# Performance work log

Measured on AMD Instinct MI355X. Metric: run time of the kernel, lower is better.

Reference implementation:

```python
import jax, jax.numpy as jnp
import numpy as np

HIDDEN = 2048
NUM_HEADS = 16
HEAD_DIM = HIDDEN // NUM_HEADS
INIT_RANGE = 0.02


def setup_inputs() -> dict:
    key = jax.random.key(0)
    ks = jax.random.split(key, 5)
    B, S = 2, 2048
    hidden_states = jax.random.normal(ks[0], (B, S, HIDDEN), dtype=jnp.float32)
    # Linear weights stored torch-style [out, in]; biases zero-init per _init_weights
    def w(k):
        return INIT_RANGE * jax.random.normal(k, (HIDDEN, HIDDEN), dtype=jnp.float32)
    return {
        "hidden_states": hidden_states,
        "wq": w(ks[1]), "bq": jnp.zeros((HIDDEN,), jnp.float32),
        "wk": w(ks[2]), "bk": jnp.zeros((HIDDEN,), jnp.float32),
        "wv": w(ks[3]), "bv": jnp.zeros((HIDDEN,), jnp.float32),
        "wo": w(ks[4]), "bo": jnp.zeros((HIDDEN,), jnp.float32),
    }


def _split_heads(x):
    # [B,S,H] -> [B,nh,S,hd]
    B, S, _ = x.shape
    return x.reshape(B, S, NUM_HEADS, HEAD_DIM).transpose(0, 2, 1, 3)


def reference(hidden_states, wq, bq, wk, bk, wv, bv, wo, bo):
    B, S, H = hidden_states.shape
    scale = 1.0 / np.sqrt(HEAD_DIM).astype(np.float32)

    q = _split_heads(hidden_states @ wq.T + bq)  # [B,nh,S,hd]
    k = _split_heads(hidden_states @ wk.T + bk)
    v = _split_heads(hidden_states @ wv.T + bv)

    attn = jnp.einsum('bhqd,bhkd->bhqk', q, k) * scale  # [B,nh,S,S]
    # causal mask: -inf above diagonal, 0 on/below
    causal = jnp.where(
        jnp.tril(jnp.ones((S, S), dtype=bool)),
        jnp.float32(0.0), jnp.float32(-jnp.inf))
    attn = attn + causal
    probs = jax.nn.softmax(attn, axis=-1)
    out = jnp.einsum('bhqk,bhkd->bhqd', probs, v)  # [B,nh,S,hd]
    out = out.transpose(0, 2, 1, 3).reshape(B, S, H)  # merge heads
    return out @ wo.T + bo
```

## Files before the change

kernel.cpp:

```cpp
#include <hip/hip_runtime.h>
#include <stdint.h>

typedef unsigned short u16;
typedef __attribute__((ext_vector_type(8))) short short8;
typedef __attribute__((ext_vector_type(4))) short short4v;
typedef __attribute__((ext_vector_type(4))) float float4v;

union V8u { short8 v; short4v h[2]; u16 u[8]; unsigned w[4]; };

__device__ __forceinline__ u16 f2bf(float f) {
  unsigned u = __float_as_uint(f);
  u = u + 0x7FFFu + ((u >> 16) & 1u);
  return (u16)(u >> 16);
}
__device__ __forceinline__ float4v fzero() {
  float4v z = {0.f, 0.f, 0.f, 0.f};
  return z;
}
__device__ __forceinline__ void gl_lds16(const u16* g, u16* l) {
  __builtin_amdgcn_global_load_lds(
      (const __attribute__((address_space(1))) void*)g,
      (__attribute__((address_space(3))) void*)l, 16, 0, 0);
}

#define MFMA16(a, b, c) __builtin_amdgcn_mfma_f32_16x16x32_bf16((a), (b), (c), 0, 0, 0)

__global__ void conv5_f32_bf16(const float* __restrict__ X,
                               const float* __restrict__ w0,
                               const float* __restrict__ w1,
                               const float* __restrict__ w2,
                               u16* __restrict__ dst, long seg) {
  const int y = blockIdx.y;
  const float* s = (y < 2) ? (X + (long)y * seg)
                           : (y == 2 ? w0 : (y == 3 ? w1 : w2));
  u16* d = dst + (long)y * seg;
  const long i = ((long)blockIdx.x * 256 + threadIdx.x) * 8;
  if (i >= seg) return;
  float4 a = *(const float4*)&s[i];
  float4 b = *(const float4*)&s[i + 4];
  V8u o;
  o.u[0] = f2bf(a.x); o.u[1] = f2bf(a.y); o.u[2] = f2bf(a.z); o.u[3] = f2bf(a.w);
  o.u[4] = f2bf(b.x); o.u[5] = f2bf(b.y); o.u[6] = f2bf(b.z); o.u[7] = f2bf(b.w);
  *(short8*)&d[i] = o.v;
}

__global__ void conv_f32_bf16(const float* __restrict__ in, u16* __restrict__ out, long n) {
  const long i = ((long)blockIdx.x * 256 + threadIdx.x) * 8;
  if (i >= n) return;
  float4 a = *(const float4*)&in[i];
  float4 b = *(const float4*)&in[i + 4];
  V8u o;
  o.u[0] = f2bf(a.x); o.u[1] = f2bf(a.y); o.u[2] = f2bf(a.z); o.u[3] = f2bf(a.w);
  o.u[4] = f2bf(b.x); o.u[5] = f2bf(b.y); o.u[6] = f2bf(b.z); o.u[7] = f2bf(b.w);
  *(short8*)&out[i] = o.v;
}

template <int NREP, bool OUTF32>
__global__ __launch_bounds__(512, 2) void gemm_bal(
    const u16* __restrict__ X, const u16* __restrict__ Wb,
    const float* __restrict__ b0, const float* __restrict__ b1,
    const float* __restrict__ b2, void* __restrict__ Out,
    int K, int cpx)
{
  constexpr int NH = NREP / 2;
  __shared__ __align__(16) u16 lds[2][(2 + NREP) * 4096];

  const int t = threadIdx.x;
  const int lane = t & 63;
  const int wave = t >> 6;
  const int quad = lane >> 4, l16 = lane & 15;
  const int wm = wave >> 2, wn = wave & 3;

  const int bid = (int)blockIdx.x;
  const int swz = (bid & 7) * cpx + (bid >> 3);
  const int by = swz & 31;
  const int bx = swz >> 5;
  const long m0 = (long)by * 128;
  const long n0 = (long)bx * (64 * NREP);

  const u16* pA[2];
  #pragma unroll
  for (int l = 0; l < 2; ++l) {
    const int d = l * 8192 + t * 16;
    const int o = d ^ ((d >> 3) & 0x70);
    pA[l] = X + (m0 + (o >> 7)) * (long)K + ((o & 127) >> 1);
  }
  const u16* pB[NREP];
  #pragma unroll
  for (int s = 0; s < NREP; ++s) {
    const int d = s * 8192 + t * 16;
    const int o = d ^ ((d >> 3) & 0x70);
    pB[s] = Wb + (n0 + (o >> 7)) * (long)K + ((o & 127) >> 1);
  }

  int offk[2];
  #pragma unroll
  for (int kk = 0; kk < 2; ++kk)
    offk[kk] = l16 * 128 + ((kk * 64 + quad * 16) ^ ((l16 & 7) << 4));

  float4v acc[4][NREP];
  #pragma unroll
  for (int i = 0; i < 4; ++i)
    #pragma unroll
    for (int j = 0; j < NREP; ++j) acc[i][j] = fzero();

  auto STAGE = [&](u16* Lb, int kt_) {
    #pragma unroll
    for (int l = 0; l < 2; ++l)
      gl_lds16(pA[l] + (long)kt_ * 64, Lb + l * 4096 + t * 8);
    #pragma unroll
    for (int s = 0; s < NREP; ++s)
      gl_lds16(pB[s] + (long)kt_ * 64, Lb + 8192 + s * 4096 + t * 8);
  };

#define SB() __builtin_amdgcn_sched_barrier(0)
#define BAR() do { asm volatile("s_barrier" ::: "memory"); SB(); } while (0)

  const int NT = K >> 6;

  STAGE(&lds[0][0], 0);
  asm volatile("s_waitcnt vmcnt(0)" ::: "memory");
  BAR();

  for (int kt = 0; kt < NT; ++kt) {
    const int buf = kt & 1;
    const int nkt = (kt + 1 < NT) ? kt + 1 : NT - 1;
    const char* Ab = (const char*)&lds[buf][0] + wm * 8192;
    const char* Bb = (const char*)&lds[buf][8192] + wn * (16 * NREP) * 128;

    short8 a[4][2], b[NREP][2];

    STAGE(&lds[buf ^ 1][0], nkt);

    #pragma unroll
    for (int i = 0; i < 4; ++i)
      a[i][0] = *(const short8*)(Ab + i * 2048 + offk[0]);
    #pragma unroll
    for (int j = 0; j < NH; ++j)
      b[j][0] = *(const short8*)(Bb + j * 2048 + offk[0]);
    #pragma unroll
    for (int j = NH; j < NREP; ++j)
      b[j][0] = *(const short8*)(Bb + j * 2048 + offk[0]);
    #pragma unroll
    for (int i = 0; i < 4; ++i)
      a[i][1] = *(const short8*)(Ab + i * 2048 + offk[1]);
    SB();

    __builtin_amdgcn_s_setprio(1);
    #pragma unroll
    for (int i = 0; i < 4; ++i)
      #pragma unroll
      for (int j = 0; j < NH; ++j)
        acc[i][j] = MFMA16(a[i][0], b[j][0], acc[i][j]);
    __builtin_amdgcn_s_setprio(0);
    SB();

    #pragma unroll
    for (int j = 0; j < NH; ++j)
      b[j][1] = *(const short8*)(Bb + j * 2048 + offk[1]);
    SB();

    __builtin_amdgcn_s_setprio(1);
    #pragma unroll
    for (int i = 0; i < 4; ++i)
      #pragma unroll
      for (int j = NH; j < NREP; ++j)
        acc[i][j] = MFMA16(a[i][0], b[j][0], acc[i][j]);
    __builtin_amdgcn_s_setprio(0);
    SB();

    #pragma unroll
    for (int j = NH; j < NREP; ++j)
      b[j][1] = *(const short8*)(Bb + j * 2048 + offk[1]);
    SB();

    __builtin_amdgcn_s_setprio(1);
    #pragma unroll
    for (int i = 0; i < 4; ++i)
      #pragma unroll
      for (int j = 0; j < NH; ++j)
        acc[i][j] = MFMA16(a[i][1], b[j][1], acc[i][j]);
    __builtin_amdgcn_s_setprio(0);
    SB();

    __builtin_amdgcn_s_setprio(1);
    #pragma unroll
    for (int i = 0; i < 4; ++i)
      #pragma unroll
      for (int j = NH; j < NREP; ++j)
        acc[i][j] = MFMA16(a[i][1], b[j][1], acc[i][j]);
    __builtin_amdgcn_s_setprio(0);

    asm volatile("s_waitcnt vmcnt(0)" ::: "memory");
    BAR();
  }

#undef SB
#undef BAR

  #pragma unroll
  for (int j = 0; j < NREP; ++j) {
    const int cg = (int)n0 + wn * (16 * NREP) + j * 16 + l16;
    const int z = cg >> 11, col = cg & 2047;
    const float* Bp = (z == 0) ? b0 : (z == 1 ? b1 : b2);
    const float bvv = Bp[col];
    #pragma unroll
    for (int i = 0; i < 4; ++i) {
      const long r0 = m0 + wm * 64 + i * 16 + quad * 4;
      #pragma unroll
      for (int r = 0; r < 4; ++r) {
        const long off = (long)z * (4096L * 2048) + (r0 + r) * 2048 + col;
        const float v = acc[i][j][r] + bvv;
        if (OUTF32) ((float*)Out)[off] = v;
        else        ((u16*)Out)[off] = f2bf(v);
      }
    }
  }
}

#define S_LEN 2048
#define HID   2048
#define HD    128

__global__ __launch_bounds__(256, 2) void attn_fwd(
    const u16* __restrict__ Q, const u16* __restrict__ K,
    const u16* __restrict__ V, u16* __restrict__ Ctx)
{
  __shared__ u16 Ks[2][32 * 136];
  __shared__ unsigned Vt[2][128 * 17];
  __shared__ u16 Ps[4 * 2 * 512];

  const int t = threadIdx.x;
  const int lane = t & 63, wave = t >> 6;
  const int quad = lane >> 4, l16 = lane & 15;
  const int b = blockIdx.y >> 4, h = blockIdx.y & 15;

  const long base = (long)b * S_LEN * HID + (long)h * HD;
  const u16* Qp = Q + base;
  const u16* Kp = K + base;
  const u16* Vp = V + base;
  u16* Cp = Ctx + base;

  const int sr2 = t >> 4;
  const int sc8 = (t & 15) * 8;

  short8 onesv;
  {
    V8u ou;
    #pragma unroll
    for (int j = 0; j < 8; ++j) ou.u[j] = 0x3F80;
    onesv = ou.v;
  }
  const float SC = 0.08838834764831845f * 1.4426950408889634f;

  for (int pass = 0; pass < 2; ++pass) {
    const int qb = (pass ? (int)blockIdx.x : 15 - (int)blockIdx.x) * 128;
    const int wqb = qb + wave * 32;

    short8 qf[2][4];
    #pragma unroll
    for (int g = 0; g < 2; ++g) {
      const long qr = wqb + g * 16 + l16;
      #pragma unroll
      for (int kk = 0; kk < 4; ++kk)
        qf[g][kk] = *(const short8*)&Qp[qr * HID + kk * 32 + quad * 8];
    }

    float4v o[2][9];
    #pragma unroll
    for (int g = 0; g < 2; ++g)
      #pragma unroll
      for (int i = 0; i < 9; ++i) o[g][i] = fzero();

    short8 kr0, kr1, vv0, vv1;
    {
      const long g = (long)(2 * sr2) * HID + sc8;
      kr0 = *(const short8*)&Kp[g];
      kr1 = *(const short8*)&Kp[g + HID];
      vv0 = *(const short8*)&Vp[g];
      vv1 = *(const short8*)&Vp[g + HID];
    }
    {
      *(short8*)&Ks[0][(2 * sr2) * 136 + sc8]     = kr0;
      *(short8*)&Ks[0][(2 * sr2 + 1) * 136 + sc8] = kr1;
      V8u a, c; a.v = vv0; c.v = vv1;
      #pragma unroll
      for (int j = 0; j < 8; ++j)
        Vt[0][(sc8 + j) * 17 + sr2] = (unsigned)a.u[j] | ((unsigned)c.u[j] << 16);
    }
    __syncthreads();

    const int T = (qb + 128) >> 5;
    for (int ti = 0; ti < T; ++ti) {
      const int kv0 = ti << 5;
      const int p = ti & 1;

      const bool more = (ti + 1 < T);
      if (more) {
        const long g = (long)(kv0 + 32 + 2 * sr2) * HID + sc8;
        kr0 = *(const short8*)&Kp[g];
        kr1 = *(const short8*)&Kp[g + HID];
        vv0 = *(const short8*)&Vp[g];
        vv1 = *(const short8*)&Vp[g + HID];
      }

      if (kv0 <= wqb) {
        float4v s[2][2];
        #pragma unroll
        for (int g = 0; g < 2; ++g) { s[g][0] = fzero(); s[g][1] = fzero(); }
        #pragma unroll
        for (int ni = 0; ni < 2; ++ni)
          #pragma unroll
          for (int kk = 0; kk < 4; ++kk) {
            short8 kf = *(const short8*)&Ks[p][(ni * 16 + l16) * 136 + kk * 32 + quad * 8];
            s[0][ni] = MFMA16(qf[0][kk], kf, s[0][ni]);
            s[1][ni] = MFMA16(qf[1][kk], kf, s[1][ni]);
          }

        const int pb = wave * 1024;
        #pragma unroll
        for (int g = 0; g < 2; ++g) {
          const int qrow0 = wqb + g * 16 + quad * 4;
          #pragma unroll
          for (int r = 0; r < 4; ++r) {
            float s0 = fminf(s[g][0][r] * SC, 80.f);
            float s1 = fminf(s[g][1][r] * SC, 80.f);
            if (kv0 + l16 > qrow0 + r)      s0 = -1e30f;
            if (kv0 + 16 + l16 > qrow0 + r) s1 = -1e30f;
            Ps[pb + g * 512 + (quad * 4 + r) * 32 + l16]      = f2bf(__builtin_amdgcn_exp2f(s0));
            Ps[pb + g * 512 + (quad * 4 + r) * 32 + 16 + l16] = f2bf(__builtin_amdgcn_exp2f(s1));
          }
        }
        __threadfence_block();
        short8 pf0 = *(const short8*)&Ps[pb + l16 * 32 + quad * 8];
        short8 pf1 = *(const short8*)&Ps[pb + 512 + l16 * 32 + quad * 8];

        #pragma unroll
        for (int dt = 0; dt < 8; ++dt) {
          const unsigned* vp = &Vt[p][(dt * 16 + l16) * 17 + quad * 4];
          V8u vf;
          vf.w[0] = vp[0]; vf.w[1] = vp[1]; vf.w[2] = vp[2]; vf.w[3] = vp[3];
          o[0][dt] = MFMA16(pf0, vf.v, o[0][dt]);
          o[1][dt] = MFMA16(pf1, vf.v, o[1][dt]);
        }
        o[0][8] = MFMA16(pf0, onesv, o[0][8]);
        o[1][8] = MFMA16(pf1, onesv, o[1][8]);
      }

      if (more) {
        *(short8*)&Ks[1 - p][(2 * sr2) * 136 + sc8]     = kr0;
        *(short8*)&Ks[1 - p][(2 * sr2 + 1) * 136 + sc8] = kr1;
        V8u a, c; a.v = vv0; c.v = vv1;
        #pragma unroll
        for (int j = 0; j < 8; ++j)
          Vt[1 - p][(sc8 + j) * 17 + sr2] = (unsigned)a.u[j] | ((unsigned)c.u[j] << 16);
      }
      __syncthreads();
    }

    #pragma unroll
    for (int g = 0; g < 2; ++g)
      #pragma unroll
      for (int r = 0; r < 4; ++r) {
        const float inv = 1.0f / o[g][8][r];
        const long qr = wqb + g * 16 + quad * 4 + r;
        #pragma unroll
        for (int dt = 0; dt < 8; ++dt)
          Cp[qr * HID + dt * 16 + l16] = f2bf(o[g][dt][r] * inv);
      }
  }
}

extern "C" void kernel_launch(void* const* d_in, const int* in_sizes, int n_in,
                              void* d_out, int out_size, void* d_ws, size_t ws_size,
                              hipStream_t stream) {
  const float* X  = (const float*)d_in[0];
  const float* wq = (const float*)d_in[1];
  const float* bq = (const float*)d_in[2];
  const float* wk = (const float*)d_in[3];
  const float* bk = (const float*)d_in[4];
  const float* wv = (const float*)d_in[5];
  const float* bv = (const float*)d_in[6];
  const float* wo = (const float*)d_in[7];
  const float* bo = (const float*)d_in[8];
  float* out = (float*)d_out;

  const long HSZ = 4096L * 2048;
  const long WSZ = 2048L * 2048;
  u16* Qw = (u16*)d_ws;
  u16* Kw = Qw + HSZ;
  u16* Vw = Kw + HSZ;
  u16* Xb = Vw + HSZ;
  u16* Wb = Xb + HSZ;
  u16* W0 = Wb;

  dim3 blk(256);
  conv5_f32_bf16<<<dim3((int)(WSZ / 2048), 5), blk, 0, stream>>>(X, wq, wk, wv, Xb, WSZ);

  gemm_bal<6, false><<<dim3(512), dim3(512), 0, stream>>>(
      Xb, Wb, bq, bk, bv, Qw, 2048, 64);

  attn_fwd<<<dim3(8, 32), blk, 0, stream>>>(Qw, Kw, Vw, Qw);

  conv_f32_bf16<<<(int)(WSZ / 2048), blk, 0, stream>>>(wo, W0, WSZ);
  gemm_bal<4, true><<<dim3(256), dim3(512), 0, stream>>>(
      Qw, W0, bo, bo, bo, out, 2048, 32);
}
```

Before: 391.3 us.

## Switch projection GEMM from 16x16x32 to 32x32x16 bf16 MFMA tiles

Replaces the 16x16x32 MFMA tiling in the projection GEMM with 32x32x16 MFMA instructions. The LDS fragment offsets, register fragments and epilogue row/column mapping are reworked to match. The k-loop is now split into four k16 sub-steps with interleaved LDS reads. The goal is fewer MFMA issues and fewer LDS fragment loads per output, in exchange for larger accumulators and a new epilogue write pattern.

```diff
diff --git a/kernel.cpp b/kernel.cpp
--- a/kernel.cpp
+++ b/kernel.cpp
@@ -5,6 +5,7 @@
 typedef __attribute__((ext_vector_type(8))) short short8;
 typedef __attribute__((ext_vector_type(4))) short short4v;
 typedef __attribute__((ext_vector_type(4))) float float4v;
+typedef __attribute__((ext_vector_type(16))) float float16v;
 
 union V8u { short8 v; short4v h[2]; u16 u[8]; unsigned w[4]; };
 
@@ -24,6 +25,7 @@
 }
 
 #define MFMA16(a, b, c) __builtin_amdgcn_mfma_f32_16x16x32_bf16((a), (b), (c), 0, 0, 0)
+#define MFMA32(a, b, c) __builtin_amdgcn_mfma_f32_32x32x16_bf16((a), (b), (c), 0, 0, 0)
 
 __global__ void conv5_f32_bf16(const float* __restrict__ X,
                                const float* __restrict__ w0,
@@ -62,13 +64,13 @@
     const float* __restrict__ b2, void* __restrict__ Out,
     int K, int cpx)
 {
-  constexpr int NH = NREP / 2;
+  constexpr int NF = NREP / 2;
   __shared__ __align__(16) u16 lds[2][(2 + NREP) * 4096];
 
   const int t = threadIdx.x;
   const int lane = t & 63;
   const int wave = t >> 6;
-  const int quad = lane >> 4, l16 = lane & 15;
+  const int l32 = lane & 31, kh = lane >> 5;
   const int wm = wave >> 2, wn = wave & 3;
 
   const int bid = (int)blockIdx.x;
@@ -93,16 +95,18 @@
     pB[s] = Wb + (n0 + (o >> 7)) * (long)K + ((o & 127) >> 1);
   }
 
-  int offk[2];
+  int offk[4];
   #pragma unroll
-  for (int kk = 0; kk < 2; ++kk)
-    offk[kk] = l16 * 128 + ((kk * 64 + quad * 16) ^ ((l16 & 7) << 4));
-
-  float4v acc[4][NREP];
+  for (int kk = 0; kk < 4; ++kk)
+    offk[kk] = l32 * 128 + ((((kk * 2 + kh) ^ (l32 & 7)) << 4));
+
+  float16v acc[2][NF];
   #pragma unroll
-  for (int i = 0; i < 4; ++i)
-    #pragma unroll
-    for (int j = 0; j < NREP; ++j) acc[i][j] = fzero();
+  for (int i = 0; i < 2; ++i)
+    #pragma unroll
+    for (int j = 0; j < NF; ++j)
+      #pragma unroll
+      for (int r = 0; r < 16; ++r) acc[i][j][r] = 0.f;
 
   auto STAGE = [&](u16* Lb, int kt_) {
     #pragma unroll
@@ -128,67 +132,73 @@
     const char* Ab = (const char*)&lds[buf][0] + wm * 8192;
     const char* Bb = (const char*)&lds[buf][8192] + wn * (16 * NREP) * 128;
 
-    short8 a[4][2], b[NREP][2];
+    short8 a[2][4], b[NF][4];
 
     STAGE(&lds[buf ^ 1][0], nkt);
 
     #pragma unroll
-    for (int i = 0; i < 4; ++i)
-      a[i][0] = *(const short8*)(Ab + i * 2048 + offk[0]);
-    #pragma unroll
-    for (int j = 0; j < NH; ++j)
-      b[j][0] = *(const short8*)(Bb + j * 2048 + offk[0]);
-    #pragma unroll
-    for (int j = NH; j < NREP; ++j)
-      b[j][0] = *(const short8*)(Bb + j * 2048 + offk[0]);
-    #pragma unroll
-    for (int i = 0; i < 4; ++i)
-      a[i][1] = *(const short8*)(Ab + i * 2048 + offk[1]);
+    for (int i = 0; i < 2; ++i) {
+      a[i][0] = *(const short8*)(Ab + i * 4096 + offk[0]);
+      a[i][1] = *(const short8*)(Ab + i * 4096 + offk[1]);
+    }
+    #pragma unroll
+    for (int j = 0; j < NF; ++j)
+      b[j][0] = *(const short8*)(Bb + j * 4096 + offk[0]);
     SB();
 
     __builtin_amdgcn_s_setprio(1);
     #pragma unroll
-    for (int i = 0; i < 4; ++i)
-      #pragma unroll
-      for (int j = 0; j < NH; ++j)
-        acc[i][j] = MFMA16(a[i][0], b[j][0], acc[i][j]);
+    for (int i = 0; i < 2; ++i)
+      #pragma unroll
+      for (int j = 0; j < NF; ++j)
+        acc[i][j] = MFMA32(a[i][0], b[j][0], acc[i][j]);
     __builtin_amdgcn_s_setprio(0);
     SB();
 
     #pragma unroll
-    for (int j = 0; j < NH; ++j)
-      b[j][1] = *(const short8*)(Bb + j * 2048 + offk[1]);
+    for (int j = 0; j < NF; ++j)
+      b[j][1] = *(const short8*)(Bb + j * 4096 + offk[1]);
     SB();
 
     __builtin_amdgcn_s_setprio(1);
     #pragma unroll
-    for (int i = 0; i < 4; ++i)
-      #pragma unroll
-      for (int j = NH; j < NREP; ++j)
-        acc[i][j] = MFMA16(a[i][0], b[j][0], acc[i][j]);
+    for (int i = 0; i < 2; ++i)
+      #pragma unroll
+      for (int j = 0; j < NF; ++j)
+        acc[i][j] = MFMA32(a[i][1], b[j][1], acc[i][j]);
     __builtin_amdgcn_s_setprio(0);
     SB();
 
     #pragma unroll
-    for (int j = NH; j < NREP; ++j)
-      b[j][1] = *(const short8*)(Bb + j * 2048 + offk[1]);
+    for (int i = 0; i < 2; ++i) {
+      a[i][2] = *(const short8*)(Ab + i * 4096 + offk[2]);
+      a[i][3] = *(const short8*)(Ab + i * 4096 + offk[3]);
+    }
+    #pragma unroll
+    for (int j = 0; j < NF; ++j)
+      b[j][2] = *(const short8*)(Bb + j * 4096 + offk[2]);
     SB();
 
     __builtin_amdgcn_s_setprio(1);
     #pragma unroll
-    for (int i = 0; i < 4; ++i)
-      #pragma unroll
-      for (int j = 0; j < NH; ++j)
-        acc[i][j] = MFMA16(a[i][1], b[j][1], acc[i][j]);
+    for (int i = 0; i < 2; ++i)
+      #pragma unroll
+      for (int j = 0; j < NF; ++j)
+        acc[i][j] = MFMA32(a[i][2], b[j][2], acc[i][j]);
     __builtin_amdgcn_s_setprio(0);
     SB();
 
+    #pragma unroll
+    for (int j = 0; j < NF; ++j)
+      b[j][3] = *(const short8*)(Bb + j * 4096 + offk[3]);
+    SB();
+
     __builtin_amdgcn_s_setprio(1);
     #pragma unroll
-    for (int i = 0; i < 4; ++i)
-      #pragma unroll
-      for (int j = NH; j < NREP; ++j)
-        acc[i][j] = MFMA16(a[i][1], b[j][1], acc[i][j]);
+    for (int i = 0; i < 2; ++i)
+      #pragma unroll
+      for (int j = 0; j < NF; ++j)
+        acc[i][j] = MFMA32(a[i][3], b[j][3], acc[i][j]);
     __builtin_amdgcn_s_setprio(0);
 
     asm volatile("s_waitcnt vmcnt(0)" ::: "memory");
@@ -199,18 +209,19 @@
 #undef BAR
 
   #pragma unroll
-  for (int j = 0; j < NREP; ++j) {
-    const int cg = (int)n0 + wn * (16 * NREP) + j * 16 + l16;
+  for (int j = 0; j < NF; ++j) {
+    const int cg = (int)n0 + wn * (16 * NREP) + j * 32 + l32;
     const int z = cg >> 11, col = cg & 2047;
     const float* Bp = (z == 0) ? b0 : (z == 1 ? b1 : b2);
     const float bvv = Bp[col];
     #pragma unroll
-    for (int i = 0; i < 4; ++i) {
-      const long r0 = m0 + wm * 64 + i * 16 + quad * 4;
-      #pragma unroll
-      for (int r = 0; r < 4; ++r) {
-        const long off = (long)z * (4096L * 2048) + (r0 + r) * 2048 + col;
-        const float v = acc[i][j][r] + bvv;
+    for (int i = 0; i < 2; ++i) {
+      const long r00 = m0 + wm * 64 + i * 32 + 4 * kh;
+      #pragma unroll
+      for (int reg = 0; reg < 16; ++reg) {
+        const long row = r00 + (reg & 3) + 8 * (reg >> 2);
+        const long off = (long)z * (4096L * 2048) + row * 2048 + col;
+        const float v = acc[i][j][reg] + bvv;
         if (OUTF32) ((float*)Out)[off] = v;
         else        ((u16*)Out)[off] = f2bf(v);
       }
```

Result: no change. 395.8 us (+1.1%).

## Use 256x256-tile quartered-pipeline GEMM for fused QKV projection

Applied to the files above, without the earlier changes.

Replaces the QKV projection GEMM with a new kernel that computes 256x256 output tiles over 384 blocks. Each K step is split into four MFMA phases, and the LDS staging of the next tile's A and B halves is interleaved between them using direct global-to-LDS loads and priority hints. Larger tiles raise arithmetic intensity and cut global reloads. In exchange, each block uses 128 KB of LDS and more accumulator registers, which may limit occupancy. The single-wave grid of 384 blocks can also leave compute units unevenly loaded.

```diff
diff --git a/kernel.cpp b/kernel.cpp
--- a/kernel.cpp
+++ b/kernel.cpp
@@ -55,6 +55,158 @@
   *(short8*)&out[i] = o.v;
 }
 
+__global__ __launch_bounds__(512, 2) void gemm256q(
+    const u16* __restrict__ X, const u16* __restrict__ Wb,
+    const float* __restrict__ b0, const float* __restrict__ b1,
+    const float* __restrict__ b2, u16* __restrict__ Out, int K)
+{
+  __shared__ __align__(16) u16 lds[2][4][8192];
+
+  const int t = threadIdx.x;
+  const int lane = t & 63;
+  const int wave = t >> 6;
+  const int quad = lane >> 4, l16 = lane & 15;
+  const int wm = wave >> 2, wn = wave & 3;
+
+  const int bid = (int)blockIdx.x;
+  const int swz = (bid & 7) * 48 + (bid >> 3);
+  const int by = swz & 15;
+  const int bx = swz >> 4;
+  const long m0 = (long)by * 256;
+  const long n0 = (long)bx * 256;
+
+  const u16* pH[4][2];
+  #pragma unroll
+  for (int l = 0; l < 2; ++l) {
+    const int d = l * 8192 + t * 16;
+    const int o = d ^ ((d >> 3) & 0x70);
+    const int r = o >> 7;
+    const int c = (o & 127) >> 1;
+    pH[0][l] = X  + (m0 + r) * (long)K + c;
+    pH[1][l] = X  + (m0 + 128 + r) * (long)K + c;
+    pH[2][l] = Wb + (n0 + r) * (long)K + c;
+    pH[3][l] = Wb + (n0 + 128 + r) * (long)K + c;
+  }
+
+  int offk[2];
+  #pragma unroll
+  for (int kk = 0; kk < 2; ++kk)
+    offk[kk] = l16 * 128 + ((kk * 64 + quad * 16) ^ ((l16 & 7) << 4));
+
+  float4v acc[8][4];
+  #pragma unroll
+  for (int i = 0; i < 8; ++i)
+    #pragma unroll
+    for (int n = 0; n < 4; ++n) acc[i][n] = fzero();
+
+  auto STG = [&](int bs, int hs, int kt_) {
+    gl_lds16(pH[hs][0] + (long)kt_ * 64, &lds[bs][hs][t * 8]);
+    gl_lds16(pH[hs][1] + (long)kt_ * 64, &lds[bs][hs][4096 + t * 8]);
+  };
+
+#define SB() __builtin_amdgcn_sched_barrier(0)
+#define BAR() do { asm volatile("s_barrier" ::: "memory"); SB(); } while (0)
+
+  const int NT = K >> 6;
+
+  STG(0, 0, 0); STG(0, 1, 0); STG(0, 2, 0); STG(0, 3, 0);
+  asm volatile("s_waitcnt vmcnt(0)" ::: "memory");
+  BAR();
+
+  for (int kt = 0; kt < NT; ++kt) {
+    const int buf = kt & 1, nb = buf ^ 1;
+    const int k1 = (kt + 1 < NT) ? kt + 1 : NT - 1;
+    const char* Ab = (const char*)&lds[buf][wm][0];
+    const char* Bb = (const char*)&lds[buf][2 + (wn >> 1)][0] + (wn & 1) * 8192;
+
+    short8 a[4], b[4];
+
+    STG(nb, 2, k1);
+    STG(nb, 3, k1);
+    #pragma unroll
+    for (int i = 0; i < 4; ++i)
+      a[i] = *(const short8*)(Ab + i * 2048 + offk[0]);
+    #pragma unroll
+    for (int n = 0; n < 4; ++n)
+      b[n] = *(const short8*)(Bb + n * 2048 + offk[0]);
+    BAR();
+    __builtin_amdgcn_s_setprio(1);
+    #pragma unroll
+    for (int i = 0; i < 4; ++i)
+      #pragma unroll
+      for (int n = 0; n < 4; ++n)
+        acc[i][n] = MFMA16(a[i], b[n], acc[i][n]);
+    __builtin_amdgcn_s_setprio(0);
+    asm volatile("s_waitcnt vmcnt(4)" ::: "memory");
+    BAR();
+
+    STG(nb, 0, k1);
+    STG(nb, 1, k1);
+    #pragma unroll
+    for (int i = 0; i < 4; ++i)
+      a[i] = *(const short8*)(Ab + (4 + i) * 2048 + offk[0]);
+    BAR();
+    __builtin_amdgcn_s_setprio(1);
+    #pragma unroll
+    for (int i = 0; i < 4; ++i)
+      #pragma unroll
+      for (int n = 0; n < 4; ++n)
+        acc[4 + i][n] = MFMA16(a[i], b[n], acc[4 + i][n]);
+    __builtin_amdgcn_s_setprio(0);
+    BAR();
+
+    #pragma unroll
+    for (int i = 0; i < 4; ++i)
+      a[i] = *(const short8*)(Ab + i * 2048 + offk[1]);
+    #pragma unroll
+    for (int n = 0; n < 4; ++n)
+      b[n] = *(const short8*)(Bb + n * 2048 + offk[1]);
+    BAR();
+    __builtin_amdgcn_s_setprio(1);
+    #pragma unroll
+    for (int i = 0; i < 4; ++i)
+      #pragma unroll
+      for (int n = 0; n < 4; ++n)
+        acc[i][n] = MFMA16(a[i], b[n], acc[i][n]);
+    __builtin_amdgcn_s_setprio(0);
+    BAR();
+
+    #pragma unroll
+    for (int i = 0; i < 4; ++i)
+      a[i] = *(const short8*)(Ab + (4 + i) * 2048 + offk[1]);
+    BAR();
+    __builtin_amdgcn_s_setprio(1);
+    #pragma unroll
+    for (int i = 0; i < 4; ++i)
+      #pragma unroll
+      for (int n = 0; n < 4; ++n)
+        acc[4 + i][n] = MFMA16(a[i], b[n], acc[4 + i][n]);
+    __builtin_amdgcn_s_setprio(0);
+    asm volatile("s_waitcnt vmcnt(2)" ::: "memory");
+    BAR();
+  }
+  asm volatile("s_waitcnt vmcnt(0)" ::: "memory");
+
+#undef SB
+#undef BAR
+
+  #pragma unroll
+  for (int n = 0; n < 4; ++n) {
+    const int cg = (int)n0 + wn * 64 + n * 16 + l16;
+    const int z = cg >> 11, col = cg & 2047;
+    const float* Bp = (z == 0) ? b0 : (z == 1 ? b1 : b2);
+    const float bvv = Bp[col];
+    #pragma unroll
+    for (int i = 0; i < 8; ++i) {
+      const long r0 = m0 + wm * 128 + i * 16 + quad * 4;
+      #pragma unroll
+      for (int r = 0; r < 4; ++r)
+        Out[(long)z * (4096L * 2048) + (r0 + r) * 2048 + col] =
+            f2bf(acc[i][n][r] + bvv);
+    }
+  }
+}
+
 template <int NREP, bool OUTF32>
 __global__ __launch_bounds__(512, 2) void gemm_bal(
     const u16* __restrict__ X, const u16* __restrict__ Wb,
@@ -397,8 +549,8 @@
   dim3 blk(256);
   conv5_f32_bf16<<<dim3((int)(WSZ / 2048), 5), blk, 0, stream>>>(X, wq, wk, wv, Xb, WSZ);
 
-  gemm_bal<6, false><<<dim3(512), dim3(512), 0, stream>>>(
-      Xb, Wb, bq, bk, bv, Qw, 2048, 64);
+  gemm256q<<<dim3(384), dim3(512), 0, stream>>>(
+      Xb, Wb, bq, bk, bv, Qw, 2048);
 
   attn_fwd<<<dim3(8, 32), blk, 0, stream>>>(Qw, Kw, Vw, Qw);
 
```

New measurement: 412.1 us. +5.3%, slower.
